# Performance work log

Measured on AMD Instinct MI355X. Metric: run time of the kernel, lower is better.

## Reference

```python
import jax, jax.numpy as jnp
import numpy as np

EPS = 1e-5
K_NUM, EDGE_TYPE = 5, 2  # k_num = A_fixed_partitions(3) + edge_type(2)


def _bn(x, gamma, beta):
    # training-mode BatchNorm2d: batch stats over (N, T, V) per channel
    m = jnp.mean(x, axis=(0, 2, 3), keepdims=True)
    v = jnp.var(x, axis=(0, 2, 3), keepdims=True)
    return (x - m) * jax.lax.rsqrt(v + EPS) * gamma[None, :, None, None] + beta[None, :, None, None]


def setup_inputs() -> dict:
    key = jax.random.key(0)
    ks = jax.random.split(key, 6)
    N, C, T, V = 32, 64, 300, 25
    Cout, Kt = 64, 9
    x = jax.random.normal(ks[0], (N, C, T, V), jnp.float32)
    A = jax.random.uniform(ks[1], (K_NUM - EDGE_TYPE, V, V), jnp.float32) / V  # fixed adjacency (already scaled by edge_importance)
    B = jax.random.uniform(ks[2], (N, EDGE_TYPE, V, V), jnp.float32) / V      # per-sample adaptive adjacency A_act
    lamda_act = jnp.full((1,), 0.5, jnp.float32)
    conv_w = jax.random.normal(ks[3], (Cout * K_NUM, C), jnp.float32) * (1.0 / np.sqrt(C))  # 1x1 conv weight
    conv_b = jnp.zeros((Cout * K_NUM,), jnp.float32)
    bn1_g = jnp.ones((Cout,), jnp.float32)
    bn1_b = jnp.zeros((Cout,), jnp.float32)
    tcn_w = jax.random.normal(ks[4], (Cout, Cout, Kt, 1), jnp.float32) * (1.0 / np.sqrt(Cout * Kt))
    tcn_b = jnp.zeros((Cout,), jnp.float32)
    bn2_g = jnp.ones((Cout,), jnp.float32)
    bn2_b = jnp.zeros((Cout,), jnp.float32)
    return dict(x=x, A=A, B=B, lamda_act=lamda_act, conv_w=conv_w, conv_b=conv_b,
                bn1_g=bn1_g, bn1_b=bn1_b, tcn_w=tcn_w, tcn_b=tcn_b, bn2_g=bn2_g, bn2_b=bn2_b)


def reference(x, A, B, lamda_act, conv_w, conv_b, bn1_g, bn1_b, tcn_w, tcn_b, bn2_g, bn2_b):
    n, c, t, v = x.shape
    res = x  # identity residual (in_ch == out_ch, stride 1)
    # SpatialGcn: 1x1 conv (pure channel GEMM) -> split -> dual einsum graph conv
    y = jnp.einsum('nctv,oc->notv', x, conv_w) + conv_b[None, :, None, None]  # (n, K*Cout, t, v)
    cout = y.shape[1] // K_NUM
    y = y.reshape(n, K_NUM, cout, t, v)
    x1 = jnp.einsum('nkctv,kvw->nctw', y[:, :K_NUM - EDGE_TYPE], A)   # fixed adjacency
    x2 = jnp.einsum('nkctv,nkvw->nctw', y[:, K_NUM - EDGE_TYPE:], B)  # adaptive adjacency
    g = x1 + x2 * lamda_act[0]
    # tcn: BN -> ReLU -> temporal conv (9,1) pad (4,0) -> BN -> Dropout(0)=identity
    h = jax.nn.relu(_bn(g, bn1_g, bn1_b))
    h = jax.lax.conv_general_dilated(h, tcn_w, window_strides=(1, 1),
                                     padding=((4, 4), (0, 0)),
                                     dimension_numbers=('NCHW', 'OIHW', 'NCHW'))
    h = h + tcn_b[None, :, None, None]
    h = _bn(h, bn2_g, bn2_b)
    return jax.nn.relu(h + res)
```

## Files before the change

### kernel.cpp

```cpp
#include <hip/hip_runtime.h>
#include <hip/hip_bf16.h>

#define N_  32
#define C_  64
#define T_  300
#define V_  25
#define TV  (T_*V_)
#define CTV (C_*TV)
#define NELEM (N_*CTV)
#define CNTF 240000.0f

typedef float f32x4 __attribute__((ext_vector_type(4)));
typedef short bf16x8 __attribute__((ext_vector_type(8)));
typedef short s4v __attribute__((ext_vector_type(4)));
typedef short s8v __attribute__((ext_vector_type(8)));

__device__ __forceinline__ unsigned short f2bf(float f) {
    unsigned u = __float_as_uint(f);
    unsigned r = u + 0x7fffu + ((u >> 16) & 1u);
    return (unsigned short)(r >> 16);
}
__device__ __forceinline__ float bf2f(unsigned short u) {
    return __uint_as_float(((unsigned)u) << 16);
}
__device__ __forceinline__ unsigned cvt_pk(float lo, float hi) {
    unsigned r;
    asm("v_cvt_pk_bf16_f32 %0, %1, %2" : "=v"(r) : "v"(lo), "v"(hi));
    return r;
}

__global__ __launch_bounds__(256) void k_prep(
    const float* __restrict__ conv_w, const float* __restrict__ tw,
    const float* __restrict__ A,
    unsigned short* __restrict__ w2b, unsigned short* __restrict__ twb,
    unsigned short* __restrict__ ashA)
{
    int tid = blockIdx.x*256 + threadIdx.x;
    for (int e = tid; e < 20480; e += 8192) {
        int ks = e >> 11, c = (e >> 5) & 63, kk = e & 31;
        w2b[e] = f2bf(conv_w[(((ks>>1)*64 + c)*64) + (ks&1)*32 + kk]);
    }
    for (int e = tid; e < 36864; e += 8192) {
        int gi = e >> 11, c = (e >> 5) & 63, kk = e & 31;
        int dt = gi >> 1, ks = gi & 1;
        twb[e] = f2bf(tw[(c*64 + 32*ks + kk)*9 + dt]);
    }
    for (int e = tid; e < 3840; e += 8192) {
        int k = e / 1280, r = e - k*1280, w = r / 40, v = r % 40;
        float val = (w < 25 && v < 25) ? A[k*625 + v*25 + w] : 0.f;
        ashA[e] = f2bf(val);
    }
}

__global__ __launch_bounds__(256) void k_prepn(
    const float* __restrict__ A, const float* __restrict__ B,
    const float* __restrict__ lamda,
    unsigned short* __restrict__ bshB, float* __restrict__ csumN)
{
    const int n = blockIdx.x, tid = threadIdx.x;
    const float lam = lamda[0];
    unsigned short* dst = bshB + n*2560;
    {
        s8v z8 = {0,0,0,0,0,0,0,0};
        for (int e = tid; e < 320; e += 256) *(s8v*)&dst[e*8] = z8;
    }
    __syncthreads();
    for (int e = tid; e < 1250; e += 256) {
        int k = e / 625, r = e - k*625, v = r / 25, w = r - v*25;
        dst[k*1280 + w*40 + v] = f2bf(lam * B[((n<<1) + k)*625 + r]);
    }
    for (int e = tid; e < 160; e += 256) {
        int k = e / 32, w = e % 32;
        float s = 0.f;
        if (w < 25) {
            if (k < 3) { for (int v = 0; v < 25; ++v) s += bf2f(f2bf(A[k*625 + v*25 + w])); }
            else       { for (int v = 0; v < 25; ++v) s += bf2f(f2bf(lam * B[((n<<1)+(k-3))*625 + v*25 + w])); }
        }
        csumN[n*160 + e] = s;
    }
}

__global__ __launch_bounds__(256) void k_gcn(
    const float* __restrict__ x,
    const unsigned short* __restrict__ ashA, const unsigned short* __restrict__ bshB,
    const float* __restrict__ csumN,
    const unsigned short* __restrict__ w2b, const float* __restrict__ conv_b,
    unsigned short* __restrict__ gout, float* __restrict__ stats3)
{
    __shared__ unsigned short zsh[10496];

    const int tb = blockIdx.x, n = blockIdx.y;
    const int t0 = tb*5;
    const int tid = threadIdx.x;
    const int lane = tid & 63, wv = tid >> 6;
    const int lg = lane >> 4, lr = lane & 15;
    const int crow = lr + 16*wv;
    const int cbase = 16*wv + 4*lg;

    bf16x8 wfrag[10];
    #pragma unroll
    for (int ks = 0; ks < 10; ++ks)
        wfrag[ks] = *(const bf16x8*)&w2b[(ks*64 + crow)*32 + 8*lg];

    const float* csum = csumN + n*160;
    float bs0[4], bs1[4];
    #pragma unroll
    for (int r = 0; r < 4; ++r) {
        float s0 = 0.f, s1 = 0.f;
        #pragma unroll
        for (int k = 0; k < 5; ++k) {
            float cb = conv_b[k*64 + cbase + r];
            s0 += cb * csum[k*32 + lr];
            s1 += cb * csum[k*32 + lr + 16];
        }
        bs0[r] = s0; bs1[r] = s1;
    }

    float sacc[4] = {0,0,0,0}, qacc[4] = {0,0,0,0};

    const float* xrow = x + n*CTV + crow*TV + t0*V_;
    float xf[8];
    #pragma unroll
    for (int i = 0; i < 8; ++i) { int v = 8*lg + i; xf[i] = (v < 25) ? xrow[v] : 0.f; }

    for (int tl = 0; tl < 5; ++tl) {
        union { bf16x8 v; unsigned u[4]; } xu;
        #pragma unroll
        for (int p = 0; p < 4; ++p) xu.u[p] = cvt_pk(xf[2*p], xf[2*p+1]);
        bf16x8 xfrag = xu.v;
        if (tl < 4) {
            const float* xn = xrow + (tl+1)*V_;
            #pragma unroll
            for (int i = 0; i < 8; ++i) { int v = 8*lg + i; xf[i] = (v < 25) ? xn[v] : 0.f; }
        }
        #pragma unroll
        for (int k = 0; k < 5; ++k)
        #pragma unroll
        for (int nt = 0; nt < 2; ++nt) {
            const unsigned short* asrc = (k < 3) ? (ashA + k*1280)
                                                 : (bshB + n*2560 + (k-3)*1280);
            bf16x8 bfrag = *(const bf16x8*)&asrc[(lr + 16*nt)*40 + 8*lg];
            f32x4 z = {0.f,0.f,0.f,0.f};
            z = __builtin_amdgcn_mfma_f32_16x16x32_bf16(xfrag, bfrag, z, 0, 0, 0);
            uint2 zz;
            zz.x = cvt_pk(z[0], z[1]);
            zz.y = cvt_pk(z[2], z[3]);
            *(uint2*)&zsh[(lr + 16*nt)*328 + k*64 + 16*wv + 4*lg] = zz;
        }
        __syncthreads();
        f32x4 acc0 = {0.f,0.f,0.f,0.f}, acc1 = {0.f,0.f,0.f,0.f};
        #pragma unroll
        for (int ks = 0; ks < 10; ++ks) {
            bf16x8 b0 = *(const bf16x8*)&zsh[lr*328 + 32*ks + 8*lg];
            bf16x8 b1 = *(const bf16x8*)&zsh[(lr+16)*328 + 32*ks + 8*lg];
            acc0 = __builtin_amdgcn_mfma_f32_16x16x32_bf16(wfrag[ks], b0, acc0, 0, 0, 0);
            acc1 = __builtin_amdgcn_mfma_f32_16x16x32_bf16(wfrag[ks], b1, acc1, 0, 0, 0);
        }
        float v0a[4], v1a[4];
        #pragma unroll
        for (int r = 0; r < 4; ++r) {
            v0a[r] = acc0[r] + bs0[r];
            v1a[r] = acc1[r] + bs1[r];
            sacc[r] += v0a[r] + (lr < 9 ? v1a[r] : 0.f);
            qacc[r] += v0a[r]*v0a[r] + (lr < 9 ? v1a[r]*v1a[r] : 0.f);
        }
        unsigned short* grow = gout + (size_t)(n*300 + t0 + tl)*1600;
        uint2 g0, g1;
        g0.x = cvt_pk(v0a[0], v0a[1]); g0.y = cvt_pk(v0a[2], v0a[3]);
        g1.x = cvt_pk(v1a[0], v1a[1]); g1.y = cvt_pk(v1a[2], v1a[3]);
        *(uint2*)&grow[lr*64 + cbase] = g0;
        if (lr < 9) *(uint2*)&grow[(lr+16)*64 + cbase] = g1;
        __syncthreads();
    }

    #pragma unroll
    for (int r = 0; r < 4; ++r) {
        float s = sacc[r], q = qacc[r];
        s += __shfl_xor(s, 1); s += __shfl_xor(s, 2);
        s += __shfl_xor(s, 4); s += __shfl_xor(s, 8);
        q += __shfl_xor(q, 1); q += __shfl_xor(q, 2);
        q += __shfl_xor(q, 4); q += __shfl_xor(q, 8);
        if (lr == 0) {
            stats3[(n*60 + tb)*128 + cbase + r] = s;
            stats3[(n*60 + tb)*128 + 64 + cbase + r] = q;
        }
    }
}

__global__ __launch_bounds__(256) void k_fin(
    const float* __restrict__ src, int count, float* __restrict__ sbo,
    const float* __restrict__ gma, const float* __restrict__ bta)
{
    const int c = blockIdx.x, tid = threadIdx.x;
    float s = 0.f, q = 0.f;
    for (int b = tid; b < count; b += 256) {
        s += src[b*128 + c];
        q += src[b*128 + 64 + c];
    }
    #pragma unroll
    for (int m = 1; m < 64; m <<= 1) { s += __shfl_xor(s, m); q += __shfl_xor(q, m); }
    __shared__ float rs[4], rq[4];
    if ((tid & 63) == 0) { rs[tid>>6] = s; rq[tid>>6] = q; }
    __syncthreads();
    if (tid == 0) {
        s = rs[0]+rs[1]+rs[2]+rs[3]; q = rq[0]+rq[1]+rq[2]+rq[3];
        float mean = s / CNTF, var = q / CNTF - mean*mean;
        float sc = gma[c] * rsqrtf(var + 1e-5f);
        sbo[c] = sc;
        sbo[64 + c] = bta[c] - mean*sc;
    }
}

__global__ __launch_bounds__(256) void k_tcn(
    const unsigned short* __restrict__ g, const float* __restrict__ sb,
    const unsigned short* __restrict__ twb, const float* __restrict__ tb,
    unsigned short* __restrict__ hout, float* __restrict__ stats4)
{
    __shared__ unsigned short lds[328*64];
    __shared__ float sbs[128];

    const int bj = blockIdx.x, n = blockIdx.y;
    const int j0 = bj*128;
    const int tid = threadIdx.x;
    const int lane = tid & 63, ct = tid >> 6;
    const int lg = lane >> 4, lr = lane & 15;
    const int cA = ct*16 + lr;
    const int cbase = ct*16 + 4*lg;

    if (tid < 128) sbs[tid] = sb[tid];
    __syncthreads();

    for (int e = tid; e < 2624; e += 256) {
        int row = e >> 3, q = e & 7;
        int gr = j0 - 100 + row;
        uint4 pk4 = {0,0,0,0};
        if (gr >= 0 && gr < 7500) {
            s8v raw = *(const s8v*)&g[((size_t)n*7500 + gr)*64 + q*8];
            float f[8];
            #pragma unroll
            for (int j = 0; j < 8; ++j)
                f[j] = fmaxf(fmaf(bf2f((unsigned short)raw[j]), sbs[q*8+j], sbs[64+q*8+j]), 0.f);
            pk4.x = cvt_pk(f[0], f[1]);
            pk4.y = cvt_pk(f[2], f[3]);
            pk4.z = cvt_pk(f[4], f[5]);
            pk4.w = cvt_pk(f[6], f[7]);
        }
        *(uint4*)&lds[row*64 + ((q ^ (row & 7)))*8] = pk4;
    }

    f32x4 acc[8];
    #pragma unroll
    for (int i = 0; i < 8; ++i) acc[i] = (f32x4){0.f,0.f,0.f,0.f};
    float tbc[4];
    #pragma unroll
    for (int r = 0; r < 4; ++r) tbc[r] = tb[cbase + r];

    __syncthreads();

    #pragma unroll
    for (int ks = 0; ks < 2; ++ks) {
        bf16x8 af[9];
        #pragma unroll
        for (int dt = 0; dt < 9; ++dt)
            af[dt] = *(const bf16x8*)&twb[((2*dt + ks)*64 + cA)*32 + 8*lg];
        #pragma unroll
        for (int jt = 0; jt < 8; ++jt) {
            #pragma unroll
            for (int dt = 0; dt < 9; ++dt) {
                int row = 16*jt + lr + 25*dt;
                bf16x8 b = *(const bf16x8*)&lds[row*64 + ((4*ks + lg) ^ (row & 7))*8];
                acc[jt] = __builtin_amdgcn_mfma_f32_16x16x32_bf16(af[dt], b, acc[jt], 0, 0, 0);
            }
        }
    }

    float sacc[4] = {0,0,0,0}, qacc[4] = {0,0,0,0};
    #pragma unroll
    for (int jt = 0; jt < 8; ++jt) {
        int j = j0 + 16*jt + lr;
        if (j < 7500) {
            #pragma unroll
            for (int r = 0; r < 4; ++r) {
                float v = acc[jt][r] + tbc[r];
                sacc[r] += v; qacc[r] += v*v;
            }
        }
    }
    #pragma unroll
    for (int r = 0; r < 4; ++r) {
        float s = sacc[r], q = qacc[r];
        s += __shfl_xor(s, 1); s += __shfl_xor(s, 2);
        s += __shfl_xor(s, 4); s += __shfl_xor(s, 8);
        q += __shfl_xor(q, 1); q += __shfl_xor(q, 2);
        q += __shfl_xor(q, 4); q += __shfl_xor(q, 8);
        if (lr == 0) {
            float* dst = stats4 + (size_t)(n*59 + bj)*128;
            dst[cbase + r] = s;
            dst[64 + cbase + r] = q;
        }
    }

    __syncthreads();
    #pragma unroll
    for (int jt = 0; jt < 8; ++jt)
        #pragma unroll
        for (int r = 0; r < 4; ++r)
            lds[(cbase + r)*136 + 16*jt + lr] = f2bf(acc[jt][r] + tbc[r]);
    __syncthreads();
    for (int e = tid; e < 2048; e += 256) {
        int row = e >> 5, c4 = (e & 31) << 2;
        int j = j0 + c4;
        if (j < 7500)
            *(s4v*)&hout[(size_t)(n*64 + row)*7500 + j] = *(const s4v*)&lds[row*136 + c4];
    }
}

__global__ __launch_bounds__(256) void k_out(
    const unsigned short* __restrict__ h, const float* __restrict__ x,
    const float* __restrict__ sb, float* __restrict__ out)
{
    int i4 = blockIdx.x * 256 + threadIdx.x;
    if (i4 >= NELEM/4) return;
    int c = ((i4*4) / TV) & 63;
    float s2 = sb[128 + c], b2 = sb[192 + c];
    s4v hv = *(const s4v*)&h[i4*4];
    float4 xv = ((const float4*)x)[i4];
    float4 o;
    o.x = fmaxf(fmaf(bf2f((unsigned short)hv[0]), s2, b2) + xv.x, 0.f);
    o.y = fmaxf(fmaf(bf2f((unsigned short)hv[1]), s2, b2) + xv.y, 0.f);
    o.z = fmaxf(fmaf(bf2f((unsigned short)hv[2]), s2, b2) + xv.z, 0.f);
    o.w = fmaxf(fmaf(bf2f((unsigned short)hv[3]), s2, b2) + xv.w, 0.f);
    ((float4*)out)[i4] = o;
}

extern "C" void kernel_launch(void* const* d_in, const int* in_sizes, int n_in,
                              void* d_out, int out_size, void* d_ws, size_t ws_size,
                              hipStream_t stream)
{
    const float* x      = (const float*)d_in[0];
    const float* A      = (const float*)d_in[1];
    const float* B      = (const float*)d_in[2];
    const float* lamda  = (const float*)d_in[3];
    const float* conv_w = (const float*)d_in[4];
    const float* conv_b = (const float*)d_in[5];
    const float* bn1_g  = (const float*)d_in[6];
    const float* bn1_b  = (const float*)d_in[7];
    const float* tcn_w  = (const float*)d_in[8];
    const float* tcn_b  = (const float*)d_in[9];
    const float* bn2_g  = (const float*)d_in[10];
    const float* bn2_b  = (const float*)d_in[11];

    unsigned short* g = (unsigned short*)d_ws;
    unsigned short* h = g + NELEM;
    float* stats3 = (float*)(h + NELEM);
    float* stats4 = stats3 + 1920*128;
    float* sb     = stats4 + 1888*128;
    float* csumN  = sb + 256;
    unsigned short* w2b  = (unsigned short*)(csumN + 32*160);
    unsigned short* twb  = w2b + 20480;
    unsigned short* ashA = twb + 36864;
    unsigned short* bshB = ashA + 3840;

    k_prep<<<32, 256, 0, stream>>>(conv_w, tcn_w, A, w2b, twb, ashA);
    k_prepn<<<32, 256, 0, stream>>>(A, B, lamda, bshB, csumN);
    k_gcn<<<dim3(60, N_), 256, 0, stream>>>(x, ashA, bshB, csumN, w2b, conv_b, g, stats3);
    k_fin<<<64, 256, 0, stream>>>(stats3, 1920, sb, bn1_g, bn1_b);
    k_tcn<<<dim3(59, N_), 256, 0, stream>>>(g, sb, twb, tcn_b, h, stats4);
    k_fin<<<64, 256, 0, stream>>>(stats4, 1888, sb + 128, bn2_g, bn2_b);
    k_out<<<NELEM/4/256, 256, 0, stream>>>(h, x, sb, (float*)d_out);
}
```

Baseline: 144.3 us.

## Process two time steps per iteration in k_gcn and stage adjacency in LDS

Each k_gcn block now covers 10 time steps instead of 5 and handles two time steps per loop iteration, using a double-sized LDS z buffer. This halves the number of barriers per time step and increases MFMA work between syncs. The adjacency fragments (A and per-sample B) are first copied into shared memory instead of being read from global memory on every iteration. The grid halves to 960 blocks, which lowers occupancy across the CUs and raises LDS usage per block. The stats buffer and the k_fin count are adjusted to match.

```diff
diff --git a/kernel.cpp b/kernel.cpp
--- a/kernel.cpp
+++ b/kernel.cpp
@@ -87,10 +87,11 @@
     const unsigned short* __restrict__ w2b, const float* __restrict__ conv_b,
     unsigned short* __restrict__ gout, float* __restrict__ stats3)
 {
-    __shared__ unsigned short zsh[10496];
+    __shared__ unsigned short ash[6400];
+    __shared__ unsigned short zsh[2][10496];
 
     const int tb = blockIdx.x, n = blockIdx.y;
-    const int t0 = tb*5;
+    const int t0 = tb*10;
     const int tid = threadIdx.x;
     const int lane = tid & 63, wv = tid >> 6;
     const int lg = lane >> 4, lr = lane & 15;
@@ -102,6 +103,11 @@
     for (int ks = 0; ks < 10; ++ks)
         wfrag[ks] = *(const bf16x8*)&w2b[(ks*64 + crow)*32 + 8*lg];
 
+    for (int e = tid; e < 480; e += 256)
+        *(s8v*)&ash[e*8] = *(const s8v*)&ashA[e*8];
+    for (int e = tid; e < 320; e += 256)
+        *(s8v*)&ash[3840 + e*8] = *(const s8v*)&bshB[n*2560 + e*8];
+
     const float* csum = csumN + n*160;
     float bs0[4], bs1[4];
     #pragma unroll
@@ -119,57 +125,82 @@
     float sacc[4] = {0,0,0,0}, qacc[4] = {0,0,0,0};
 
     const float* xrow = x + n*CTV + crow*TV + t0*V_;
-    float xf[8];
-    #pragma unroll
-    for (int i = 0; i < 8; ++i) { int v = 8*lg + i; xf[i] = (v < 25) ? xrow[v] : 0.f; }
-
-    for (int tl = 0; tl < 5; ++tl) {
-        union { bf16x8 v; unsigned u[4]; } xu;
-        #pragma unroll
-        for (int p = 0; p < 4; ++p) xu.u[p] = cvt_pk(xf[2*p], xf[2*p+1]);
-        bf16x8 xfrag = xu.v;
-        if (tl < 4) {
-            const float* xn = xrow + (tl+1)*V_;
+    float xf0[8], xf1[8];
+    #pragma unroll
+    for (int i = 0; i < 8; ++i) {
+        int v = 8*lg + i;
+        xf0[i] = (v < 25) ? xrow[v] : 0.f;
+        xf1[i] = (v < 25) ? xrow[V_ + v] : 0.f;
+    }
+
+    __syncthreads();
+
+    for (int tp = 0; tp < 5; ++tp) {
+        union { bf16x8 v; unsigned u[4]; } xu0, xu1;
+        #pragma unroll
+        for (int p = 0; p < 4; ++p) {
+            xu0.u[p] = cvt_pk(xf0[2*p], xf0[2*p+1]);
+            xu1.u[p] = cvt_pk(xf1[2*p], xf1[2*p+1]);
+        }
+        bf16x8 xg0 = xu0.v, xg1 = xu1.v;
+        if (tp < 4) {
+            const float* xn = xrow + (2*tp + 2)*V_;
             #pragma unroll
-            for (int i = 0; i < 8; ++i) { int v = 8*lg + i; xf[i] = (v < 25) ? xn[v] : 0.f; }
+            for (int i = 0; i < 8; ++i) {
+                int v = 8*lg + i;
+                xf0[i] = (v < 25) ? xn[v] : 0.f;
+                xf1[i] = (v < 25) ? xn[V_ + v] : 0.f;
+            }
         }
         #pragma unroll
         for (int k = 0; k < 5; ++k)
         #pragma unroll
         for (int nt = 0; nt < 2; ++nt) {
-            const unsigned short* asrc = (k < 3) ? (ashA + k*1280)
-                                                 : (bshB + n*2560 + (k-3)*1280);
-            bf16x8 bfrag = *(const bf16x8*)&asrc[(lr + 16*nt)*40 + 8*lg];
-            f32x4 z = {0.f,0.f,0.f,0.f};
-            z = __builtin_amdgcn_mfma_f32_16x16x32_bf16(xfrag, bfrag, z, 0, 0, 0);
-            uint2 zz;
-            zz.x = cvt_pk(z[0], z[1]);
-            zz.y = cvt_pk(z[2], z[3]);
-            *(uint2*)&zsh[(lr + 16*nt)*328 + k*64 + 16*wv + 4*lg] = zz;
+            bf16x8 bfrag = *(const bf16x8*)&ash[k*1280 + (lr + 16*nt)*40 + 8*lg];
+            f32x4 z0 = {0.f,0.f,0.f,0.f}, z1 = {0.f,0.f,0.f,0.f};
+            z0 = __builtin_amdgcn_mfma_f32_16x16x32_bf16(xg0, bfrag, z0, 0, 0, 0);
+            z1 = __builtin_amdgcn_mfma_f32_16x16x32_bf16(xg1, bfrag, z1, 0, 0, 0);
+            uint2 p0, p1;
+            p0.x = cvt_pk(z0[0], z0[1]); p0.y = cvt_pk(z0[2], z0[3]);
+            p1.x = cvt_pk(z1[0], z1[1]); p1.y = cvt_pk(z1[2], z1[3]);
+            const int zoff = (lr + 16*nt)*328 + k*64 + 16*wv + 4*lg;
+            *(uint2*)&zsh[0][zoff] = p0;
+            *(uint2*)&zsh[1][zoff] = p1;
         }
         __syncthreads();
-        f32x4 acc0 = {0.f,0.f,0.f,0.f}, acc1 = {0.f,0.f,0.f,0.f};
+        f32x4 a00 = {0.f,0.f,0.f,0.f}, a01 = {0.f,0.f,0.f,0.f};
+        f32x4 a10 = {0.f,0.f,0.f,0.f}, a11 = {0.f,0.f,0.f,0.f};
         #pragma unroll
         for (int ks = 0; ks < 10; ++ks) {
-            bf16x8 b0 = *(const bf16x8*)&zsh[lr*328 + 32*ks + 8*lg];
-            bf16x8 b1 = *(const bf16x8*)&zsh[(lr+16)*328 + 32*ks + 8*lg];
-            acc0 = __builtin_amdgcn_mfma_f32_16x16x32_bf16(wfrag[ks], b0, acc0, 0, 0, 0);
-            acc1 = __builtin_amdgcn_mfma_f32_16x16x32_bf16(wfrag[ks], b1, acc1, 0, 0, 0);
-        }
-        float v0a[4], v1a[4];
+            bf16x8 b00 = *(const bf16x8*)&zsh[0][lr*328 + 32*ks + 8*lg];
+            bf16x8 b01 = *(const bf16x8*)&zsh[0][(lr+16)*328 + 32*ks + 8*lg];
+            bf16x8 b10 = *(const bf16x8*)&zsh[1][lr*328 + 32*ks + 8*lg];
+            bf16x8 b11 = *(const bf16x8*)&zsh[1][(lr+16)*328 + 32*ks + 8*lg];
+            a00 = __builtin_amdgcn_mfma_f32_16x16x32_bf16(wfrag[ks], b00, a00, 0, 0, 0);
+            a01 = __builtin_amdgcn_mfma_f32_16x16x32_bf16(wfrag[ks], b01, a01, 0, 0, 0);
+            a10 = __builtin_amdgcn_mfma_f32_16x16x32_bf16(wfrag[ks], b10, a10, 0, 0, 0);
+            a11 = __builtin_amdgcn_mfma_f32_16x16x32_bf16(wfrag[ks], b11, a11, 0, 0, 0);
+        }
+        float v00[4], v01[4], v10[4], v11[4];
         #pragma unroll
         for (int r = 0; r < 4; ++r) {
-            v0a[r] = acc0[r] + bs0[r];
-            v1a[r] = acc1[r] + bs1[r];
-            sacc[r] += v0a[r] + (lr < 9 ? v1a[r] : 0.f);
-            qacc[r] += v0a[r]*v0a[r] + (lr < 9 ? v1a[r]*v1a[r] : 0.f);
-        }
-        unsigned short* grow = gout + (size_t)(n*300 + t0 + tl)*1600;
-        uint2 g0, g1;
-        g0.x = cvt_pk(v0a[0], v0a[1]); g0.y = cvt_pk(v0a[2], v0a[3]);
-        g1.x = cvt_pk(v1a[0], v1a[1]); g1.y = cvt_pk(v1a[2], v1a[3]);
-        *(uint2*)&grow[lr*64 + cbase] = g0;
-        if (lr < 9) *(uint2*)&grow[(lr+16)*64 + cbase] = g1;
+            v00[r] = a00[r] + bs0[r]; v01[r] = a01[r] + bs1[r];
+            v10[r] = a10[r] + bs0[r]; v11[r] = a11[r] + bs1[r];
+            sacc[r] += v00[r] + v10[r] + (lr < 9 ? v01[r] + v11[r] : 0.f);
+            qacc[r] += v00[r]*v00[r] + v10[r]*v10[r]
+                     + (lr < 9 ? v01[r]*v01[r] + v11[r]*v11[r] : 0.f);
+        }
+        unsigned short* grow0 = gout + (size_t)(n*300 + t0 + 2*tp)*1600;
+        unsigned short* grow1 = grow0 + 1600;
+        uint2 ga, gb;
+        ga.x = cvt_pk(v00[0], v00[1]); ga.y = cvt_pk(v00[2], v00[3]);
+        gb.x = cvt_pk(v01[0], v01[1]); gb.y = cvt_pk(v01[2], v01[3]);
+        *(uint2*)&grow0[lr*64 + cbase] = ga;
+        if (lr < 9) *(uint2*)&grow0[(lr+16)*64 + cbase] = gb;
+        ga.x = cvt_pk(v10[0], v10[1]); ga.y = cvt_pk(v10[2], v10[3]);
+        gb.x = cvt_pk(v11[0], v11[1]); gb.y = cvt_pk(v11[2], v11[3]);
+        *(uint2*)&grow1[lr*64 + cbase] = ga;
+        if (lr < 9) *(uint2*)&grow1[(lr+16)*64 + cbase] = gb;
         __syncthreads();
     }
 
@@ -181,8 +212,8 @@
         q += __shfl_xor(q, 1); q += __shfl_xor(q, 2);
         q += __shfl_xor(q, 4); q += __shfl_xor(q, 8);
         if (lr == 0) {
-            stats3[(n*60 + tb)*128 + cbase + r] = s;
-            stats3[(n*60 + tb)*128 + 64 + cbase + r] = q;
+            stats3[(n*30 + tb)*128 + cbase + r] = s;
+            stats3[(n*30 + tb)*128 + 64 + cbase + r] = q;
         }
     }
 }
@@ -353,7 +384,7 @@
     unsigned short* g = (unsigned short*)d_ws;
     unsigned short* h = g + NELEM;
     float* stats3 = (float*)(h + NELEM);
-    float* stats4 = stats3 + 1920*128;
+    float* stats4 = stats3 + 960*128;
     float* sb     = stats4 + 1888*128;
     float* csumN  = sb + 256;
     unsigned short* w2b  = (unsigned short*)(csumN + 32*160);
@@ -363,8 +394,8 @@
 
     k_prep<<<32, 256, 0, stream>>>(conv_w, tcn_w, A, w2b, twb, ashA);
     k_prepn<<<32, 256, 0, stream>>>(A, B, lamda, bshB, csumN);
-    k_gcn<<<dim3(60, N_), 256, 0, stream>>>(x, ashA, bshB, csumN, w2b, conv_b, g, stats3);
-    k_fin<<<64, 256, 0, stream>>>(stats3, 1920, sb, bn1_g, bn1_b);
+    k_gcn<<<dim3(30, N_), 256, 0, stream>>>(x, ashA, bshB, csumN, w2b, conv_b, g, stats3);
+    k_fin<<<64, 256, 0, stream>>>(stats3, 960, sb, bn1_g, bn1_b);
     k_tcn<<<dim3(59, N_), 256, 0, stream>>>(g, sb, twb, tcn_b, h, stats4);
     k_fin<<<64, 256, 0, stream>>>(stats4, 1888, sb + 128, bn2_g, bn2_b);
     k_out<<<NELEM/4/256, 256, 0, stream>>>(h, x, sb, (float*)d_out);
```

New measurement: 131.7 us. -8.8%, faster.

## Stage x tile, adjacency and gcn output through LDS; merge prep kernels

Applied to the files above, without the earlier changes.

The gcn kernel now loads the whole 5-timestep x tile into shared memory as bf16 up front. It also copies the fixed and adaptive adjacency fragments into LDS, pads the z staging stride to 344, and buffers the output rows in LDS so they can be written back with coalesced 16-byte stores. The k_prepn kernel is folded into k_prep, which removes one launch. The aim is better global access patterns and fewer LDS bank conflicts, at the cost of much more shared memory per block and possibly lower occupancy.

```diff
diff --git a/kernel.cpp b/kernel.cpp
--- a/kernel.cpp
+++ b/kernel.cpp
@@ -9,6 +9,7 @@
 #define CTV (C_*TV)
 #define NELEM (N_*CTV)
 #define CNTF 240000.0f
+#define ZST 344
 
 typedef float f32x4 __attribute__((ext_vector_type(4)));
 typedef short bf16x8 __attribute__((ext_vector_type(8)));
@@ -31,32 +32,27 @@
 
 __global__ __launch_bounds__(256) void k_prep(
     const float* __restrict__ conv_w, const float* __restrict__ tw,
-    const float* __restrict__ A,
+    const float* __restrict__ A, const float* __restrict__ B,
+    const float* __restrict__ lamda,
     unsigned short* __restrict__ w2b, unsigned short* __restrict__ twb,
-    unsigned short* __restrict__ ashA)
-{
-    int tid = blockIdx.x*256 + threadIdx.x;
-    for (int e = tid; e < 20480; e += 8192) {
+    unsigned short* __restrict__ ashA, unsigned short* __restrict__ bshB,
+    float* __restrict__ csumN)
+{
+    const int gtid = blockIdx.x*256 + threadIdx.x;
+    for (int e = gtid; e < 20480; e += 8192) {
         int ks = e >> 11, c = (e >> 5) & 63, kk = e & 31;
         w2b[e] = f2bf(conv_w[(((ks>>1)*64 + c)*64) + (ks&1)*32 + kk]);
     }
-    for (int e = tid; e < 36864; e += 8192) {
+    for (int e = gtid; e < 36864; e += 8192) {
         int gi = e >> 11, c = (e >> 5) & 63, kk = e & 31;
         int dt = gi >> 1, ks = gi & 1;
         twb[e] = f2bf(tw[(c*64 + 32*ks + kk)*9 + dt]);
     }
-    for (int e = tid; e < 3840; e += 8192) {
+    for (int e = gtid; e < 3840; e += 8192) {
         int k = e / 1280, r = e - k*1280, w = r / 40, v = r % 40;
         float val = (w < 25 && v < 25) ? A[k*625 + v*25 + w] : 0.f;
         ashA[e] = f2bf(val);
     }
-}
-
-__global__ __launch_bounds__(256) void k_prepn(
-    const float* __restrict__ A, const float* __restrict__ B,
-    const float* __restrict__ lamda,
-    unsigned short* __restrict__ bshB, float* __restrict__ csumN)
-{
     const int n = blockIdx.x, tid = threadIdx.x;
     const float lam = lamda[0];
     unsigned short* dst = bshB + n*2560;
@@ -87,7 +83,10 @@
     const unsigned short* __restrict__ w2b, const float* __restrict__ conv_b,
     unsigned short* __restrict__ gout, float* __restrict__ stats3)
 {
-    __shared__ unsigned short zsh[10496];
+    __shared__ unsigned short ash[6400];
+    __shared__ unsigned short zsh[32*ZST];
+    __shared__ unsigned short xsh[12800];
+    __shared__ unsigned short gsh[8000];
 
     const int tb = blockIdx.x, n = blockIdx.y;
     const int t0 = tb*5;
@@ -102,6 +101,26 @@
     for (int ks = 0; ks < 10; ++ks)
         wfrag[ks] = *(const bf16x8*)&w2b[(ks*64 + crow)*32 + 8*lg];
 
+    for (int e = tid; e < 480; e += 256)
+        *(s8v*)&ash[e*8] = *(const s8v*)&ashA[e*8];
+    for (int e = tid; e < 320; e += 256)
+        *(s8v*)&ash[3840 + e*8] = *(const s8v*)&bshB[n*2560 + e*8];
+
+    for (int e = tid; e < 1600; e += 256) {
+        int tq = e / 320, r = e - tq*320, c = r / 5, vg = r - c*5;
+        const float* xs = x + (size_t)n*CTV + c*TV + (t0 + tq)*V_ + vg*8;
+        float f[8];
+        #pragma unroll
+        for (int j = 0; j < 8; ++j) {
+            int v = vg*8 + j;
+            f[j] = (v < 25) ? xs[j] : 0.f;
+        }
+        union { s8v v; unsigned u[4]; } pk;
+        #pragma unroll
+        for (int p = 0; p < 4; ++p) pk.u[p] = cvt_pk(f[2*p], f[2*p+1]);
+        *(s8v*)&xsh[(tq*64 + c)*40 + vg*8] = pk.v;
+    }
+
     const float* csum = csumN + n*160;
     float bs0[4], bs1[4];
     #pragma unroll
@@ -118,41 +137,28 @@
 
     float sacc[4] = {0,0,0,0}, qacc[4] = {0,0,0,0};
 
-    const float* xrow = x + n*CTV + crow*TV + t0*V_;
-    float xf[8];
-    #pragma unroll
-    for (int i = 0; i < 8; ++i) { int v = 8*lg + i; xf[i] = (v < 25) ? xrow[v] : 0.f; }
+    __syncthreads();
 
     for (int tl = 0; tl < 5; ++tl) {
-        union { bf16x8 v; unsigned u[4]; } xu;
-        #pragma unroll
-        for (int p = 0; p < 4; ++p) xu.u[p] = cvt_pk(xf[2*p], xf[2*p+1]);
-        bf16x8 xfrag = xu.v;
-        if (tl < 4) {
-            const float* xn = xrow + (tl+1)*V_;
-            #pragma unroll
-            for (int i = 0; i < 8; ++i) { int v = 8*lg + i; xf[i] = (v < 25) ? xn[v] : 0.f; }
-        }
+        bf16x8 xfrag = *(const bf16x8*)&xsh[(tl*64 + crow)*40 + 8*lg];
         #pragma unroll
         for (int k = 0; k < 5; ++k)
         #pragma unroll
         for (int nt = 0; nt < 2; ++nt) {
-            const unsigned short* asrc = (k < 3) ? (ashA + k*1280)
-                                                 : (bshB + n*2560 + (k-3)*1280);
-            bf16x8 bfrag = *(const bf16x8*)&asrc[(lr + 16*nt)*40 + 8*lg];
+            bf16x8 bfrag = *(const bf16x8*)&ash[k*1280 + (lr + 16*nt)*40 + 8*lg];
             f32x4 z = {0.f,0.f,0.f,0.f};
             z = __builtin_amdgcn_mfma_f32_16x16x32_bf16(xfrag, bfrag, z, 0, 0, 0);
             uint2 zz;
             zz.x = cvt_pk(z[0], z[1]);
             zz.y = cvt_pk(z[2], z[3]);
-            *(uint2*)&zsh[(lr + 16*nt)*328 + k*64 + 16*wv + 4*lg] = zz;
+            *(uint2*)&zsh[(lr + 16*nt)*ZST + k*64 + 16*wv + 4*lg] = zz;
         }
         __syncthreads();
         f32x4 acc0 = {0.f,0.f,0.f,0.f}, acc1 = {0.f,0.f,0.f,0.f};
         #pragma unroll
         for (int ks = 0; ks < 10; ++ks) {
-            bf16x8 b0 = *(const bf16x8*)&zsh[lr*328 + 32*ks + 8*lg];
-            bf16x8 b1 = *(const bf16x8*)&zsh[(lr+16)*328 + 32*ks + 8*lg];
+            bf16x8 b0 = *(const bf16x8*)&zsh[lr*ZST + 32*ks + 8*lg];
+            bf16x8 b1 = *(const bf16x8*)&zsh[(lr+16)*ZST + 32*ks + 8*lg];
             acc0 = __builtin_amdgcn_mfma_f32_16x16x32_bf16(wfrag[ks], b0, acc0, 0, 0, 0);
             acc1 = __builtin_amdgcn_mfma_f32_16x16x32_bf16(wfrag[ks], b1, acc1, 0, 0, 0);
         }
@@ -164,13 +170,18 @@
             sacc[r] += v0a[r] + (lr < 9 ? v1a[r] : 0.f);
             qacc[r] += v0a[r]*v0a[r] + (lr < 9 ? v1a[r]*v1a[r] : 0.f);
         }
-        unsigned short* grow = gout + (size_t)(n*300 + t0 + tl)*1600;
         uint2 g0, g1;
         g0.x = cvt_pk(v0a[0], v0a[1]); g0.y = cvt_pk(v0a[2], v0a[3]);
         g1.x = cvt_pk(v1a[0], v1a[1]); g1.y = cvt_pk(v1a[2], v1a[3]);
-        *(uint2*)&grow[lr*64 + cbase] = g0;
-        if (lr < 9) *(uint2*)&grow[(lr+16)*64 + cbase] = g1;
+        *(uint2*)&gsh[tl*1600 + lr*64 + cbase] = g0;
+        if (lr < 9) *(uint2*)&gsh[tl*1600 + (lr+16)*64 + cbase] = g1;
         __syncthreads();
+    }
+
+    for (int e = tid; e < 1000; e += 256) {
+        int tq = e / 200, r = e - tq*200;
+        *(s8v*)&gout[(size_t)(n*300 + t0 + tq)*1600 + r*8] =
+            *(const s8v*)&gsh[tq*1600 + r*8];
     }
 
     #pragma unroll
@@ -361,8 +372,7 @@
     unsigned short* ashA = twb + 36864;
     unsigned short* bshB = ashA + 3840;
 
-    k_prep<<<32, 256, 0, stream>>>(conv_w, tcn_w, A, w2b, twb, ashA);
-    k_prepn<<<32, 256, 0, stream>>>(A, B, lamda, bshB, csumN);
+    k_prep<<<32, 256, 0, stream>>>(conv_w, tcn_w, A, B, lamda, w2b, twb, ashA, bshB, csumN);
     k_gcn<<<dim3(60, N_), 256, 0, stream>>>(x, ashA, bshB, csumN, w2b, conv_b, g, stats3);
     k_fin<<<64, 256, 0, stream>>>(stats3, 1920, sb, bn1_g, bn1_b);
     k_tcn<<<dim3(59, N_), 256, 0, stream>>>(g, sb, twb, tcn_b, h, stats4);
```

Result: slower. 152.1 us (+5.4%).
